# Kernel optimization log

Hardware: AMD Instinct MI355X
Metric: run time of the kernel (lower is better)

The kernel has to match this reference:

```python
import jax, jax.numpy as jnp
import numpy as np

D_MODEL = 768
N_HEADS = 12
D_HEAD = D_MODEL // N_HEADS
D_FF = 3072
LN_EPS = 1e-5


def setup_inputs() -> dict:
    key = jax.random.key(0)
    ks = jax.random.split(key, 16)
    B, L = 2, 2048
    s = 0.02
    inp = {
        "x": jax.random.normal(ks[0], (B, L, D_MODEL), jnp.float32),
        "Wq": jax.random.normal(ks[1], (D_MODEL, D_MODEL), jnp.float32) * s,
        "bq": jnp.zeros((D_MODEL,), jnp.float32),
        "Wk": jax.random.normal(ks[2], (D_MODEL, D_MODEL), jnp.float32) * s,
        "bk": jnp.zeros((D_MODEL,), jnp.float32),
        "Wv": jax.random.normal(ks[3], (D_MODEL, D_MODEL), jnp.float32) * s,
        "bv": jnp.zeros((D_MODEL,), jnp.float32),
        "Wo": jax.random.normal(ks[4], (D_MODEL, D_MODEL), jnp.float32) * s,
        "bo": jnp.zeros((D_MODEL,), jnp.float32),
        "g1": jnp.ones((D_MODEL,), jnp.float32),
        "b1": jnp.zeros((D_MODEL,), jnp.float32),
        "g2": jnp.ones((D_MODEL,), jnp.float32),
        "b2": jnp.zeros((D_MODEL,), jnp.float32),
        "W1": jax.random.normal(ks[5], (D_FF, D_MODEL), jnp.float32) * s,
        "c1": jnp.zeros((D_FF,), jnp.float32),
        "W2": jax.random.normal(ks[6], (D_MODEL, D_FF), jnp.float32) * s,
        "c2": jnp.zeros((D_MODEL,), jnp.float32),
        "is_causal": 1,
    }
    return inp


def _layernorm(x, g, b):
    mu = jnp.mean(x, axis=-1, keepdims=True)
    var = jnp.mean(jnp.square(x - mu), axis=-1, keepdims=True)
    return (x - mu) * jax.lax.rsqrt(var + LN_EPS) * g + b


def _mha(xn, Wq, bq, Wk, bk, Wv, bv, Wo, bo, is_causal):
    B, L, D = xn.shape
    q = (xn @ Wq.T + bq).reshape(B, L, N_HEADS, D_HEAD)
    k = (xn @ Wk.T + bk).reshape(B, L, N_HEADS, D_HEAD)
    v = (xn @ Wv.T + bv).reshape(B, L, N_HEADS, D_HEAD)
    scale = D_HEAD ** -0.5
    # [B, H, Lq, Lk] full score matrix (faithful to naive implementation)
    scores = jnp.einsum("bqhd,bkhd->bhqk", q, k) * scale
    if is_causal:
        mask = jnp.triu(jnp.ones((L, L), dtype=bool), k=1)
        scores = jnp.where(mask, -jnp.inf, scores)
    attn = jax.nn.softmax(scores, axis=-1)
    out = jnp.einsum("bhqk,bkhd->bqhd", attn, v).reshape(B, L, D)
    return out @ Wo.T + bo


def reference(x, Wq, bq, Wk, bk, Wv, bv, Wo, bo, g1, b1, g2, b2, W1, c1, W2, c2, is_causal):
    # pre-norm block, dropout=0 (eval)
    normed = _layernorm(x, g1, b1)
    x = x + _mha(normed, Wq, bq, Wk, bk, Wv, bv, Wo, bo, is_causal)
    normed = _layernorm(x, g2, b2)
    h = jax.nn.gelu(normed @ W1.T + c1, approximate=False)
    x = x + (h @ W2.T + c2)
    return x
```

## Files before the change

kernel.cpp:

```cpp
#include <hip/hip_runtime.h>

typedef __attribute__((ext_vector_type(8))) __bf16 bf16x8;
typedef __attribute__((ext_vector_type(4))) __bf16 bf16x4;
typedef __attribute__((ext_vector_type(4))) float f32x4;

#define D_MODEL 768
#define D_FF    3072
#define NT      4096
#define NH      12
#define DH      64
#define LBATCH  2048
#define LDQKV   2304
#define NQT     32
#define NCHUNK  4

__device__ __forceinline__ f32x4 mfma16(bf16x8 a, bf16x8 b, f32x4 c) {
  return __builtin_amdgcn_mfma_f32_16x16x32_bf16(a, b, c, 0, 0, 0);
}

__device__ __forceinline__ void gl_lds16(const __bf16* g, __bf16* l) {
  __builtin_amdgcn_global_load_lds(
      (const __attribute__((address_space(1))) void*)g,
      (__attribute__((address_space(3))) void*)l, 16, 0, 0);
}

struct ConvArgs {
  const float* src[6];
  __bf16* dst[6];
  int n4[6];
};

__global__ __launch_bounds__(256) void conv_kernel(ConvArgs a) {
  const int m = blockIdx.y;
  const int i = blockIdx.x * 256 + threadIdx.x;
  if (i < a.n4[m]) {
    float4 v = ((const float4*)a.src[m])[i];
    bf16x4 o = {(__bf16)v.x, (__bf16)v.y, (__bf16)v.z, (__bf16)v.w};
    ((bf16x4*)a.dst[m])[i] = o;
  }
}

__global__ __launch_bounds__(256) void ln_kernel(const float* __restrict__ x,
                                                 const float* __restrict__ g,
                                                 const float* __restrict__ b,
                                                 __bf16* __restrict__ out) {
  const int row  = blockIdx.x * 4 + (threadIdx.x >> 6);
  const int lane = threadIdx.x & 63;
  const float4* xr = (const float4*)(x + (size_t)row * D_MODEL + lane * 12);
  float v[12];
  float4 a0 = xr[0], a1 = xr[1], a2 = xr[2];
  v[0] = a0.x; v[1] = a0.y; v[2]  = a0.z; v[3]  = a0.w;
  v[4] = a1.x; v[5] = a1.y; v[6]  = a1.z; v[7]  = a1.w;
  v[8] = a2.x; v[9] = a2.y; v[10] = a2.z; v[11] = a2.w;
  float s = 0.f;
#pragma unroll
  for (int i = 0; i < 12; ++i) s += v[i];
#pragma unroll
  for (int o = 32; o > 0; o >>= 1) s += __shfl_xor(s, o, 64);
  const float mean = s * (1.0f / 768.0f);
  float vs = 0.f;
#pragma unroll
  for (int i = 0; i < 12; ++i) { float d = v[i] - mean; vs += d * d; }
#pragma unroll
  for (int o = 32; o > 0; o >>= 1) vs += __shfl_xor(vs, o, 64);
  const float rstd = rsqrtf(vs * (1.0f / 768.0f) + 1e-5f);
  const int col0 = lane * 12;
#pragma unroll
  for (int i = 0; i < 12; ++i) {
    float gv = g[col0 + i], bv = b[col0 + i];
    out[(size_t)row * D_MODEL + col0 + i] = (__bf16)((v[i] - mean) * rstd * gv + bv);
  }
}

template <int BN, int EPI, typename OutT>
__global__ __launch_bounds__(256) void gemm_bt(const __bf16* __restrict__ A,
                                               const __bf16* __restrict__ W,
                                               const float* __restrict__ bias,
                                               const float* __restrict__ biasK,
                                               const float* __restrict__ biasV,
                                               const float* __restrict__ res,
                                               OutT* __restrict__ C,
                                               int M, int N, int K) {
  constexpr int WN = (BN == 128) ? 2 : 1;
  constexpr int WM = 4 / WN;
  constexpr int MROWS = 128 / WM;
  constexpr int MF = MROWS / 16;
  constexpr int NF = (BN / WN) / 16;
  __shared__ __bf16 As[128 * 64];
  __shared__ __bf16 Bs[BN * 64];
  const int tid = threadIdx.x;
  const int lane = tid & 63, w = tid >> 6;
  const int wr = w / WN, wc = w % WN;
  const int l15 = lane & 15, l4 = lane >> 4;
  const int m0 = blockIdx.y * 128, n0 = blockIdx.x * BN;

  f32x4 acc[MF][NF];
#pragma unroll
  for (int i = 0; i < MF; ++i)
#pragma unroll
    for (int j = 0; j < NF; ++j) acc[i][j] = f32x4{0.f, 0.f, 0.f, 0.f};

  const int srow = tid >> 3;
  const int sblk = tid & 7;

  for (int k0 = 0; k0 < K; k0 += 64) {
    __syncthreads();
#pragma unroll
    for (int i = 0; i < 4; ++i) {
      const int row = i * 32 + srow;
      gl_lds16(A + (size_t)(m0 + row) * K + k0 + ((sblk ^ ((row & 1) << 2)) << 3),
               &As[(row * 8 + sblk) * 8]);
    }
#pragma unroll
    for (int i = 0; i < BN / 32; ++i) {
      const int row = i * 32 + srow;
      gl_lds16(W + (size_t)(n0 + row) * K + k0 + ((sblk ^ ((row & 1) << 2)) << 3),
               &Bs[(row * 8 + sblk) * 8]);
    }
    __syncthreads();
#pragma unroll
    for (int kk = 0; kk < 2; ++kk) {
      const int poff = ((((kk ^ (l15 & 1)) << 2) | l4) << 3);
      bf16x8 a[MF], bf[NF];
#pragma unroll
      for (int mf = 0; mf < MF; ++mf)
        a[mf] = *(const bf16x8*)(&As[(wr * MROWS + mf * 16 + l15) * 64 + poff]);
#pragma unroll
      for (int nf = 0; nf < NF; ++nf)
        bf[nf] = *(const bf16x8*)(&Bs[(wc * 64 + nf * 16 + l15) * 64 + poff]);
#pragma unroll
      for (int mf = 0; mf < MF; ++mf)
#pragma unroll
        for (int nf = 0; nf < NF; ++nf)
          acc[mf][nf] = mfma16(a[mf], bf[nf], acc[mf][nf]);
    }
  }

#pragma unroll
  for (int mf = 0; mf < MF; ++mf)
#pragma unroll
    for (int nf = 0; nf < NF; ++nf) {
      const int col = n0 + wc * 64 + nf * 16 + l15;
      float bcol;
      if constexpr (EPI == 3)
        bcol = (col < 768) ? bias[col] : (col < 1536 ? biasK[col - 768] : biasV[col - 1536]);
      else
        bcol = bias[col];
#pragma unroll
      for (int r = 0; r < 4; ++r) {
        const int row = m0 + wr * MROWS + mf * 16 + l4 * 4 + r;
        float vv = acc[mf][nf][r] + bcol;
        if constexpr (EPI == 1) vv = 0.5f * vv * (1.0f + erff(vv * 0.70710678118f));
        if constexpr (EPI == 2) vv += res[(size_t)row * N + col];
        C[(size_t)row * N + col] = (OutT)vv;
      }
    }
}

__global__ __launch_bounds__(256) void attn_part(const __bf16* __restrict__ qkv,
                                                 const int* __restrict__ is_causal,
                                                 __bf16* __restrict__ Opn,
                                                 float* __restrict__ Ml) {
  const int qt = blockIdx.x >> 2, ch = blockIdx.x & 3;
  const int h = blockIdx.y, bb = blockIdx.z;
  const int causal = *is_causal;
  const int nkt = causal ? (qt + 1) : NQT;
  const int kt0 = ch * 8;
  if (kt0 >= nkt) return;
  const int ktEnd = (kt0 + 8 < nkt) ? (kt0 + 8) : nkt;

  __shared__ __bf16 Ks[2][64 * 64];
  __shared__ __bf16 Vt[2][64 * 72];
  __shared__ __bf16 Ps[64 * 72];
  const int tid = threadIdx.x, lane = tid & 63, w = tid >> 6;
  const int l15 = lane & 15, l4 = lane >> 4, l15b = l15 >> 3;
  const size_t rowbase = (size_t)bb * LBATCH;

  const int sr0 = tid >> 3, sr1 = 32 + (tid >> 3), sdb = tid & 7;
  const int hs0 = (((sr0 >> 3) & 1) << 2) | (sr0 >> 4);
  const int hs1 = (((sr1 >> 3) & 1) << 2) | (sr1 >> 4);
  const int kofs0 = ((sdb ^ hs0) << 3);
  const int kofs1 = ((sdb ^ hs1) << 3);
  const int gv = (((sdb & 1) << 2) | (sdb >> 1));
  const int vcol0 = (((sr0 >> 3) ^ gv) << 3) + (sr0 & 7);
  const int vcol1 = (((sr1 >> 3) ^ gv) << 3) + (sr1 & 7);
  const size_t kvrow0 = (rowbase)*LDQKV;

  const __bf16* qp = qkv + (rowbase + qt * 64 + w * 16 + l15) * LDQKV + h * DH;
  bf16x8 bq0 = *(const bf16x8*)(qp + l4 * 8);
  bf16x8 bq1 = *(const bf16x8*)(qp + 32 + l4 * 8);

  f32x4 oacc[4];
#pragma unroll
  for (int df = 0; df < 4; ++df) oacc[df] = f32x4{0.f, 0.f, 0.f, 0.f};
  float mrun = -__builtin_inff(), lrun = 0.f;

  {
    const size_t g0 = (rowbase + kt0 * 64 + sr0) * LDQKV + h * DH;
    const size_t g1 = (rowbase + kt0 * 64 + sr1) * LDQKV + h * DH;
    gl_lds16(qkv + g0 + 768 + kofs0, &Ks[0][sr0 * 64 + sdb * 8]);
    gl_lds16(qkv + g1 + 768 + kofs1, &Ks[0][sr1 * 64 + sdb * 8]);
    bf16x8 v0 = *(const bf16x8*)(qkv + g0 + 1536 + sdb * 8);
    bf16x8 v1 = *(const bf16x8*)(qkv + g1 + 1536 + sdb * 8);
#pragma unroll
    for (int j = 0; j < 8; ++j) {
      Vt[0][(sdb * 8 + j) * 72 + vcol0] = v0[j];
      Vt[0][(sdb * 8 + j) * 72 + vcol1] = v1[j];
    }
  }
  __syncthreads();

  int cur = 0;
  for (int kt = kt0; kt < ktEnd; ++kt, cur ^= 1) {
    const bool pf = (kt + 1 < ktEnd);
    bf16x8 pv0, pv1;
    if (pf) {
      const size_t g0 = (rowbase + (kt + 1) * 64 + sr0) * LDQKV + h * DH;
      const size_t g1 = (rowbase + (kt + 1) * 64 + sr1) * LDQKV + h * DH;
      gl_lds16(qkv + g0 + 768 + kofs0, &Ks[cur ^ 1][sr0 * 64 + sdb * 8]);
      gl_lds16(qkv + g1 + 768 + kofs1, &Ks[cur ^ 1][sr1 * 64 + sdb * 8]);
      pv0 = *(const bf16x8*)(qkv + g0 + 1536 + sdb * 8);
      pv1 = *(const bf16x8*)(qkv + g1 + 1536 + sdb * 8);
    }

    f32x4 sacc[4];
    __builtin_amdgcn_s_setprio(1);
#pragma unroll
    for (int nf = 0; nf < 4; ++nf) {
      const int krow = nf * 16 + l15;
      const int pb = (l4 ^ nf);
      bf16x8 ka0 = *(const bf16x8*)(&Ks[cur][krow * 64 + ((((0 ^ l15b) << 2) | pb) << 3)]);
      bf16x8 ka1 = *(const bf16x8*)(&Ks[cur][krow * 64 + ((((1 ^ l15b) << 2) | pb) << 3)]);
      sacc[nf] = mfma16(ka0, bq0, f32x4{0.f, 0.f, 0.f, 0.f});
      sacc[nf] = mfma16(ka1, bq1, sacc[nf]);
    }
    __builtin_amdgcn_s_setprio(0);

    float p[4][4];
    float mx = -__builtin_inff();
#pragma unroll
    for (int nf = 0; nf < 4; ++nf)
#pragma unroll
      for (int r = 0; r < 4; ++r) {
        float sv = sacc[nf][r] * 0.125f;
        if (causal && kt == qt && (nf * 16 + l4 * 4 + r) > (w * 16 + l15))
          sv = -__builtin_inff();
        p[nf][r] = sv;
        mx = fmaxf(mx, sv);
      }
    mx = fmaxf(mx, __shfl_xor(mx, 16, 64));
    mx = fmaxf(mx, __shfl_xor(mx, 32, 64));
    const float mnew = fmaxf(mrun, mx);
    float sum = 0.f;
#pragma unroll
    for (int nf = 0; nf < 4; ++nf)
#pragma unroll
      for (int r = 0; r < 4; ++r) {
        float pe = __expf(p[nf][r] - mnew);
        p[nf][r] = pe;
        sum += pe;
      }
    sum += __shfl_xor(sum, 16, 64);
    sum += __shfl_xor(sum, 32, 64);
    const float fac = __expf(mrun - mnew);
    lrun = lrun * fac + sum;
    mrun = mnew;

#pragma unroll
    for (int nf = 0; nf < 4; ++nf) {
      bf16x4 pk = {(__bf16)p[nf][0], (__bf16)p[nf][1], (__bf16)p[nf][2], (__bf16)p[nf][3]};
      *(bf16x4*)(&Ps[(w * 16 + l15) * 72 + nf * 16 + l4 * 4]) = pk;
    }

#pragma unroll
    for (int df = 0; df < 4; ++df) {
      f32x4 t = oacc[df];
#pragma unroll
      for (int r = 0; r < 4; ++r) t[r] *= fac;
      oacc[df] = t;
    }

    __builtin_amdgcn_s_setprio(1);
#pragma unroll
    for (int kk = 0; kk < 2; ++kk) {
      bf16x8 pb = *(const bf16x8*)(&Ps[(w * 16 + l15) * 72 + kk * 32 + l4 * 8]);
#pragma unroll
      for (int df = 0; df < 4; ++df) {
        const int d = df * 16 + l15;
        const int pblk = (((kk ^ l15b) << 2) | (l4 ^ df));
        bf16x8 va = *(const bf16x8*)(&Vt[cur][d * 72 + pblk * 8]);
        oacc[df] = mfma16(va, pb, oacc[df]);
      }
    }
    __builtin_amdgcn_s_setprio(0);

    if (pf) {
#pragma unroll
      for (int j = 0; j < 8; ++j) {
        Vt[cur ^ 1][(sdb * 8 + j) * 72 + vcol0] = pv0[j];
        Vt[cur ^ 1][(sdb * 8 + j) * 72 + vcol1] = pv1[j];
      }
    }
    __syncthreads();
  }

  const size_t slot = ((((size_t)bb * NH + h) << 5) + qt) * 4 + ch;
  const int ql = w * 16 + l15;
  if (l4 == 0) {
    Ml[slot * 128 + ql] = mrun;
    Ml[slot * 128 + 64 + ql] = lrun;
  }
  const float inv = 1.0f / lrun;
#pragma unroll
  for (int df = 0; df < 4; ++df) {
    bf16x4 ok = {(__bf16)(oacc[df][0] * inv), (__bf16)(oacc[df][1] * inv),
                 (__bf16)(oacc[df][2] * inv), (__bf16)(oacc[df][3] * inv)};
    *(bf16x4*)(&Opn[slot * 4096 + (size_t)ql * 64 + df * 16 + l4 * 4]) = ok;
  }
}

__global__ __launch_bounds__(256) void attn_comb(const __bf16* __restrict__ Opn,
                                                 const float* __restrict__ Ml,
                                                 const int* __restrict__ is_causal,
                                                 __bf16* __restrict__ out) {
  const int qt = blockIdx.x, h = blockIdx.y, bb = blockIdx.z;
  const int nkt = (*is_causal) ? (qt + 1) : NQT;
  const int nc = (nkt + 7) >> 3;
  const int r = threadIdx.x >> 2;
  const int d0 = (threadIdx.x & 3) * 16;
  const size_t slot0 = ((((size_t)bb * NH + h) << 5) + qt) * 4;

  float mv[4], lv[4];
  float M = -__builtin_inff();
#pragma unroll
  for (int c = 0; c < 4; ++c) {
    mv[c] = -__builtin_inff(); lv[c] = 0.f;
    if (c < nc) {
      mv[c] = Ml[(slot0 + c) * 128 + r];
      lv[c] = Ml[(slot0 + c) * 128 + 64 + r];
      M = fmaxf(M, mv[c]);
    }
  }
  float L = 0.f, wgt[4];
#pragma unroll
  for (int c = 0; c < 4; ++c) {
    wgt[c] = (c < nc) ? lv[c] * __expf(mv[c] - M) : 0.f;
    L += wgt[c];
  }
  const float invL = 1.0f / L;
  float o[16];
#pragma unroll
  for (int j = 0; j < 16; ++j) o[j] = 0.f;
#pragma unroll
  for (int c = 0; c < 4; ++c) {
    if (c < nc) {
      const float wv = wgt[c] * invL;
      const bf16x8* op = (const bf16x8*)(Opn + (slot0 + c) * 4096 + (size_t)r * 64 + d0);
      bf16x8 v0 = op[0], v1 = op[1];
#pragma unroll
      for (int j = 0; j < 8; ++j) { o[j] += wv * (float)v0[j]; o[8 + j] += wv * (float)v1[j]; }
    }
  }
  bf16x8 s0, s1;
#pragma unroll
  for (int j = 0; j < 8; ++j) { s0[j] = (__bf16)o[j]; s1[j] = (__bf16)o[8 + j]; }
  __bf16* po = out + ((size_t)bb * LBATCH + qt * 64 + r) * D_MODEL + h * DH + d0;
  *(bf16x8*)(po) = s0;
  *(bf16x8*)(po + 8) = s1;
}

extern "C" void kernel_launch(void* const* d_in, const int* in_sizes, int n_in,
                              void* d_out, int out_size, void* d_ws, size_t ws_size,
                              hipStream_t stream) {
  const float* x  = (const float*)d_in[0];
  const float* Wq = (const float*)d_in[1];
  const float* bq = (const float*)d_in[2];
  const float* Wk = (const float*)d_in[3];
  const float* bk = (const float*)d_in[4];
  const float* Wv = (const float*)d_in[5];
  const float* bv = (const float*)d_in[6];
  const float* Wo = (const float*)d_in[7];
  const float* bo = (const float*)d_in[8];
  const float* g1 = (const float*)d_in[9];
  const float* b1 = (const float*)d_in[10];
  const float* g2 = (const float*)d_in[11];
  const float* b2 = (const float*)d_in[12];
  const float* W1 = (const float*)d_in[13];
  const float* c1 = (const float*)d_in[14];
  const float* W2 = (const float*)d_in[15];
  const float* c2 = (const float*)d_in[16];
  const int* is_causal = (const int*)d_in[17];
  float* out = (float*)d_out;

  char* ws = (char*)d_ws;
  size_t off = 0;
  __bf16* xn   = (__bf16*)(ws + off); off += (size_t)NT * D_MODEL * 2;
  __bf16* qkv  = (__bf16*)(ws + off); off += (size_t)NT * LDQKV * 2;
  __bf16* hb   = (__bf16*)(ws + off); off += (size_t)NT * D_FF * 2;
  float*  x1   = (float*)(ws + off);  off += (size_t)NT * D_MODEL * 4;
  __bf16* Wqkvb = (__bf16*)(ws + off); off += (size_t)3 * D_MODEL * D_MODEL * 2;
  __bf16* Wob  = (__bf16*)(ws + off); off += (size_t)D_MODEL * D_MODEL * 2;
  __bf16* W1b  = (__bf16*)(ws + off); off += (size_t)D_FF * D_MODEL * 2;
  __bf16* W2b  = (__bf16*)(ws + off); off += (size_t)D_MODEL * D_FF * 2;
  __bf16* Opn = hb;
  float*  Ml  = x1;

  ConvArgs ca;
  ca.src[0] = Wq; ca.dst[0] = Wqkvb;                     ca.n4[0] = D_MODEL * D_MODEL / 4;
  ca.src[1] = Wk; ca.dst[1] = Wqkvb + D_MODEL * D_MODEL; ca.n4[1] = D_MODEL * D_MODEL / 4;
  ca.src[2] = Wv; ca.dst[2] = Wqkvb + 2 * D_MODEL * D_MODEL; ca.n4[2] = D_MODEL * D_MODEL / 4;
  ca.src[3] = Wo; ca.dst[3] = Wob;                       ca.n4[3] = D_MODEL * D_MODEL / 4;
  ca.src[4] = W1; ca.dst[4] = W1b;                       ca.n4[4] = D_FF * D_MODEL / 4;
  ca.src[5] = W2; ca.dst[5] = W2b;                       ca.n4[5] = D_MODEL * D_FF / 4;

  dim3 blk(256);
  dim3 gconv((D_FF * D_MODEL / 4 + 255) / 256, 6);

  conv_kernel<<<gconv, blk, 0, stream>>>(ca);
  ln_kernel<<<NT / 4, blk, 0, stream>>>(x, g1, b1, xn);
  gemm_bt<128, 3, __bf16><<<dim3(LDQKV / 128, NT / 128), blk, 0, stream>>>(
      xn, Wqkvb, bq, bk, bv, nullptr, qkv, NT, LDQKV, D_MODEL);
  attn_part<<<dim3(NQT * NCHUNK, NH, 2), blk, 0, stream>>>(qkv, is_causal, Opn, Ml);
  attn_comb<<<dim3(NQT, NH, 2), blk, 0, stream>>>(Opn, Ml, is_causal, xn);
  gemm_bt<64, 2, float><<<dim3(D_MODEL / 64, NT / 128), blk, 0, stream>>>(
      xn, Wob, bo, nullptr, nullptr, x, x1, NT, D_MODEL, D_MODEL);
  ln_kernel<<<NT / 4, blk, 0, stream>>>(x1, g2, b2, xn);
  gemm_bt<128, 1, __bf16><<<dim3(D_FF / 128, NT / 128), blk, 0, stream>>>(
      xn, W1b, c1, nullptr, nullptr, nullptr, hb, NT, D_FF, D_MODEL);
  gemm_bt<64, 2, float><<<dim3(D_MODEL / 64, NT / 128), blk, 0, stream>>>(
      hb, W2b, c2, nullptr, nullptr, x1, out, NT, D_MODEL, D_FF);
}
```

Before: 234.8 us.

## Load K directly into registers, widen LDS swizzles, add occupancy hint

The attention kernel now reads K fragments straight from global memory into registers instead of staging them in double-buffered shared memory. This frees LDS and removes the K staging traffic. The GEMM and V-transpose swizzles switch to a full 8-way XOR pattern to reduce LDS bank conflicts. Launch bounds request 4 blocks per SM for the attention kernel, and the causal mask is split out into its own branch. The K loads are now issued without prefetch, so global latency may be exposed at the start of each tile.

Measured after the change: 246.2 us. 1.05x slower.

```diff
diff --git a/kernel.cpp b/kernel.cpp
--- a/kernel.cpp
+++ b/kernel.cpp
@@ -108,19 +108,19 @@
 #pragma unroll
     for (int i = 0; i < 4; ++i) {
       const int row = i * 32 + srow;
-      gl_lds16(A + (size_t)(m0 + row) * K + k0 + ((sblk ^ ((row & 1) << 2)) << 3),
+      gl_lds16(A + (size_t)(m0 + row) * K + k0 + ((sblk ^ (row & 7)) << 3),
                &As[(row * 8 + sblk) * 8]);
     }
 #pragma unroll
     for (int i = 0; i < BN / 32; ++i) {
       const int row = i * 32 + srow;
-      gl_lds16(W + (size_t)(n0 + row) * K + k0 + ((sblk ^ ((row & 1) << 2)) << 3),
+      gl_lds16(W + (size_t)(n0 + row) * K + k0 + ((sblk ^ (row & 7)) << 3),
                &Bs[(row * 8 + sblk) * 8]);
     }
     __syncthreads();
 #pragma unroll
     for (int kk = 0; kk < 2; ++kk) {
-      const int poff = ((((kk ^ (l15 & 1)) << 2) | l4) << 3);
+      const int poff = (((kk * 4 + l4) ^ (l15 & 7)) << 3);
       bf16x8 a[MF], bf[NF];
 #pragma unroll
       for (int mf = 0; mf < MF; ++mf)
@@ -157,10 +157,10 @@
     }
 }
 
-__global__ __launch_bounds__(256) void attn_part(const __bf16* __restrict__ qkv,
-                                                 const int* __restrict__ is_causal,
-                                                 __bf16* __restrict__ Opn,
-                                                 float* __restrict__ Ml) {
+__global__ __launch_bounds__(256, 4) void attn_part(const __bf16* __restrict__ qkv,
+                                                    const int* __restrict__ is_causal,
+                                                    __bf16* __restrict__ Opn,
+                                                    float* __restrict__ Ml) {
   const int qt = blockIdx.x >> 2, ch = blockIdx.x & 3;
   const int h = blockIdx.y, bb = blockIdx.z;
   const int causal = *is_causal;
@@ -169,85 +169,84 @@
   if (kt0 >= nkt) return;
   const int ktEnd = (kt0 + 8 < nkt) ? (kt0 + 8) : nkt;
 
-  __shared__ __bf16 Ks[2][64 * 64];
   __shared__ __bf16 Vt[2][64 * 72];
   __shared__ __bf16 Ps[64 * 72];
   const int tid = threadIdx.x, lane = tid & 63, w = tid >> 6;
   const int l15 = lane & 15, l4 = lane >> 4, l15b = l15 >> 3;
   const size_t rowbase = (size_t)bb * LBATCH;
 
-  const int sr0 = tid >> 3, sr1 = 32 + (tid >> 3), sdb = tid & 7;
-  const int hs0 = (((sr0 >> 3) & 1) << 2) | (sr0 >> 4);
-  const int hs1 = (((sr1 >> 3) & 1) << 2) | (sr1 >> 4);
-  const int kofs0 = ((sdb ^ hs0) << 3);
-  const int kofs1 = ((sdb ^ hs1) << 3);
-  const int gv = (((sdb & 1) << 2) | (sdb >> 1));
-  const int vcol0 = (((sr0 >> 3) ^ gv) << 3) + (sr0 & 7);
-  const int vcol1 = (((sr1 >> 3) ^ gv) << 3) + (sr1 & 7);
-  const size_t kvrow0 = (rowbase)*LDQKV;
+  const int sr0 = tid >> 3, sr1 = 32 + sr0, sdb = tid & 7;
+  const int vc0 = (((sr0 >> 3) ^ sdb) << 3) + (sr0 & 7);
+  const int vc1 = (((sr1 >> 3) ^ sdb) << 3) + (sr1 & 7);
 
   const __bf16* qp = qkv + (rowbase + qt * 64 + w * 16 + l15) * LDQKV + h * DH;
   bf16x8 bq0 = *(const bf16x8*)(qp + l4 * 8);
   bf16x8 bq1 = *(const bf16x8*)(qp + 32 + l4 * 8);
 
+  const __bf16* kbase = qkv + (rowbase + kt0 * 64 + l15) * LDQKV + h * DH + 768 + l4 * 8;
+  const __bf16* vbase = qkv + (rowbase + kt0 * 64) * LDQKV + h * DH + 1536 + sdb * 8;
+
   f32x4 oacc[4];
 #pragma unroll
   for (int df = 0; df < 4; ++df) oacc[df] = f32x4{0.f, 0.f, 0.f, 0.f};
   float mrun = -__builtin_inff(), lrun = 0.f;
 
   {
-    const size_t g0 = (rowbase + kt0 * 64 + sr0) * LDQKV + h * DH;
-    const size_t g1 = (rowbase + kt0 * 64 + sr1) * LDQKV + h * DH;
-    gl_lds16(qkv + g0 + 768 + kofs0, &Ks[0][sr0 * 64 + sdb * 8]);
-    gl_lds16(qkv + g1 + 768 + kofs1, &Ks[0][sr1 * 64 + sdb * 8]);
-    bf16x8 v0 = *(const bf16x8*)(qkv + g0 + 1536 + sdb * 8);
-    bf16x8 v1 = *(const bf16x8*)(qkv + g1 + 1536 + sdb * 8);
+    bf16x8 v0 = *(const bf16x8*)(vbase + (size_t)sr0 * LDQKV);
+    bf16x8 v1 = *(const bf16x8*)(vbase + (size_t)sr1 * LDQKV);
 #pragma unroll
     for (int j = 0; j < 8; ++j) {
-      Vt[0][(sdb * 8 + j) * 72 + vcol0] = v0[j];
-      Vt[0][(sdb * 8 + j) * 72 + vcol1] = v1[j];
+      Vt[0][(sdb * 8 + j) * 72 + vc0] = v0[j];
+      Vt[0][(sdb * 8 + j) * 72 + vc1] = v1[j];
     }
   }
   __syncthreads();
 
   int cur = 0;
   for (int kt = kt0; kt < ktEnd; ++kt, cur ^= 1) {
+    const __bf16* kp = kbase + (size_t)(kt - kt0) * (64 * LDQKV);
+    bf16x8 ka[4][2];
+#pragma unroll
+    for (int nf = 0; nf < 4; ++nf)
+#pragma unroll
+      for (int kk = 0; kk < 2; ++kk)
+        ka[nf][kk] = *(const bf16x8*)(kp + (size_t)(nf * 16) * LDQKV + kk * 32);
+
     const bool pf = (kt + 1 < ktEnd);
     bf16x8 pv0, pv1;
     if (pf) {
-      const size_t g0 = (rowbase + (kt + 1) * 64 + sr0) * LDQKV + h * DH;
-      const size_t g1 = (rowbase + (kt + 1) * 64 + sr1) * LDQKV + h * DH;
-      gl_lds16(qkv + g0 + 768 + kofs0, &Ks[cur ^ 1][sr0 * 64 + sdb * 8]);
-      gl_lds16(qkv + g1 + 768 + kofs1, &Ks[cur ^ 1][sr1 * 64 + sdb * 8]);
-      pv0 = *(const bf16x8*)(qkv + g0 + 1536 + sdb * 8);
-      pv1 = *(const bf16x8*)(qkv + g1 + 1536 + sdb * 8);
+      const __bf16* vp = vbase + (size_t)(kt + 1 - kt0) * (64 * LDQKV);
+      pv0 = *(const bf16x8*)(vp + (size_t)sr0 * LDQKV);
+      pv1 = *(const bf16x8*)(vp + (size_t)sr1 * LDQKV);
     }
 
     f32x4 sacc[4];
     __builtin_amdgcn_s_setprio(1);
 #pragma unroll
     for (int nf = 0; nf < 4; ++nf) {
-      const int krow = nf * 16 + l15;
-      const int pb = (l4 ^ nf);
-      bf16x8 ka0 = *(const bf16x8*)(&Ks[cur][krow * 64 + ((((0 ^ l15b) << 2) | pb) << 3)]);
-      bf16x8 ka1 = *(const bf16x8*)(&Ks[cur][krow * 64 + ((((1 ^ l15b) << 2) | pb) << 3)]);
-      sacc[nf] = mfma16(ka0, bq0, f32x4{0.f, 0.f, 0.f, 0.f});
-      sacc[nf] = mfma16(ka1, bq1, sacc[nf]);
+      sacc[nf] = mfma16(ka[nf][0], bq0, f32x4{0.f, 0.f, 0.f, 0.f});
+      sacc[nf] = mfma16(ka[nf][1], bq1, sacc[nf]);
     }
     __builtin_amdgcn_s_setprio(0);
 
     float p[4][4];
+#pragma unroll
+    for (int nf = 0; nf < 4; ++nf)
+#pragma unroll
+      for (int r = 0; r < 4; ++r) p[nf][r] = sacc[nf][r] * 0.125f;
+    if (causal && kt == qt) {
+      const int wq = w * 16 + l15;
+#pragma unroll
+      for (int nf = 0; nf < 4; ++nf)
+#pragma unroll
+        for (int r = 0; r < 4; ++r)
+          if (nf * 16 + l4 * 4 + r > wq) p[nf][r] = -__builtin_inff();
+    }
     float mx = -__builtin_inff();
 #pragma unroll
     for (int nf = 0; nf < 4; ++nf)
 #pragma unroll
-      for (int r = 0; r < 4; ++r) {
-        float sv = sacc[nf][r] * 0.125f;
-        if (causal && kt == qt && (nf * 16 + l4 * 4 + r) > (w * 16 + l15))
-          sv = -__builtin_inff();
-        p[nf][r] = sv;
-        mx = fmaxf(mx, sv);
-      }
+      for (int r = 0; r < 4; ++r) mx = fmaxf(mx, p[nf][r]);
     mx = fmaxf(mx, __shfl_xor(mx, 16, 64));
     mx = fmaxf(mx, __shfl_xor(mx, 32, 64));
     const float mnew = fmaxf(mrun, mx);
@@ -287,7 +286,7 @@
 #pragma unroll
       for (int df = 0; df < 4; ++df) {
         const int d = df * 16 + l15;
-        const int pblk = (((kk ^ l15b) << 2) | (l4 ^ df));
+        const int pblk = (kk * 4 + l4) ^ (df * 2 + l15b);
         bf16x8 va = *(const bf16x8*)(&Vt[cur][d * 72 + pblk * 8]);
         oacc[df] = mfma16(va, pb, oacc[df]);
       }
@@ -297,8 +296,8 @@
     if (pf) {
 #pragma unroll
       for (int j = 0; j < 8; ++j) {
-        Vt[cur ^ 1][(sdb * 8 + j) * 72 + vcol0] = pv0[j];
-        Vt[cur ^ 1][(sdb * 8 + j) * 72 + vcol1] = pv1[j];
+        Vt[cur ^ 1][(sdb * 8 + j) * 72 + vc0] = pv0[j];
+        Vt[cur ^ 1][(sdb * 8 + j) * 72 + vc1] = pv1[j];
       }
     }
     __syncthreads();
```
